# Kernel optimization log

Measured on AMD Instinct MI355X. Metric: run time of the kernel, lower is better.

## Reference

```python
import jax, jax.numpy as jnp
import numpy as np

ALPHA = 0.2          # LeakyReLU slope
NEG_BIG = -9e15      # mask value from the torch code
LN_EPS = 1e-5        # torch LayerNorm default eps
GAT_SCALE = 1.0


def _layer_norm(x, g, b):
    mu = x.mean(-1, keepdims=True)
    var = ((x - mu) ** 2).mean(-1, keepdims=True)
    return (x - mu) * jax.lax.rsqrt(var + LN_EPS) * g + b


def _gat_layer(h, adj, W, a, concat):
    # h: [B,N,Fin], adj: [N,N] weighted, W: [Fin,Fout], a: [2*Fout,1]
    Wh = jnp.einsum('bnf,fo->bno', h, W)                 # [B,N,Fout]
    Fo = W.shape[1]
    a_i, a_j = a[:Fo, 0], a[Fo:, 0]
    # e[b,i,j] = leakyrelu(Wh[b,i].a_i + Wh[b,j].a_j)  (== cat([Wh_i,Wh_j]) @ a)
    e = jax.nn.leaky_relu(
        (Wh @ a_i)[:, :, None] + (Wh @ a_j)[:, None, :], ALPHA)  # [B,N,N]
    att = jnp.where(adj[None, :, :] > 0, e, NEG_BIG)
    att = jax.nn.softmax(att, axis=2)
    att = att * adj[None, :, :]
    att = att / (att.sum(axis=2, keepdims=True) + 1e-8)
    h_prime = jnp.einsum('bij,bjo->bio', att, Wh)        # [B,N,Fout]
    return jax.nn.elu(h_prime) if concat else h_prime


def setup_inputs() -> dict:
    B, N, H, ID = 1024, 128, 64, 8
    GIN = 1 + ID  # node_feat_dim = 0
    key = jax.random.key(0)
    ks = jax.random.split(key, 20)
    # sparse weighted adjacency with self-loops
    w = jax.random.uniform(ks[0], (N, N))
    m = (jax.random.uniform(ks[1], (N, N)) < 0.3).astype(jnp.float32)
    adj = w * m + jnp.eye(N, dtype=jnp.float32)
    sc = lambda k, s: jax.random.normal(k, s, jnp.float32) * 0.1
    return {
        'c_values': jax.random.normal(ks[2], (B, N), jnp.float32),
        'adj': adj,
        'agent_emb': sc(ks[3], (N, ID)),
        'W1': sc(ks[4], (GIN, H)), 'a1': sc(ks[5], (2 * H, 1)),
        'W2': sc(ks[6], (H, H)),   'a2': sc(ks[7], (2 * H, 1)),
        'ln1_g': jnp.ones((H,)), 'ln1_b': jnp.zeros((H,)),
        'ln2_g': jnp.ones((H,)), 'ln2_b': jnp.zeros((H,)),
        'head_gat_w': sc(ks[8], (H, 1)), 'head_gat_b': jnp.zeros((1,)),
        'mlp1_w': sc(ks[9], (N, H)),  'mlp1_b': jnp.zeros((H,)),
        'mlp2_w': sc(ks[10], (H, H)), 'mlp2_b': jnp.zeros((H,)),
        'head_mlp_w': sc(ks[11], (H, 1)), 'head_mlp_b': jnp.zeros((1,)),
        'gate1_w': sc(ks[12], (N, H)), 'gate1_b': jnp.zeros((H,)),
        'gate2_w': sc(ks[13], (H, 1)), 'gate2_b': jnp.full((1,), -5.0),
    }


def reference(c_values, adj, agent_emb, W1, a1, W2, a2,
              ln1_g, ln1_b, ln2_g, ln2_b, head_gat_w, head_gat_b,
              mlp1_w, mlp1_b, mlp2_w, mlp2_b, head_mlp_w, head_mlp_b,
              gate1_w, gate1_b, gate2_w, gate2_b):
    B, N = c_values.shape
    # node features: [c_value, agent_id_embedding]
    id_feat = jnp.broadcast_to(agent_emb[None], (B, N, agent_emb.shape[1]))
    x_g = jnp.concatenate([c_values[..., None], id_feat], axis=-1)  # [B,N,9]
    h1 = _gat_layer(x_g, adj, W1, a1, concat=True)
    h1 = _layer_norm(h1, ln1_g, ln1_b)
    h2 = _gat_layer(h1, adj, W2, a2, concat=False)
    h = jax.nn.relu(h2 + h1)
    h = _layer_norm(h, ln2_g, ln2_b)
    q_gat = h.mean(axis=1) @ head_gat_w + head_gat_b                # [B,1]
    x_m = jax.nn.relu(c_values @ mlp1_w + mlp1_b)
    x_m = jax.nn.relu(x_m @ mlp2_w + mlp2_b)
    q_mlp = x_m @ head_mlp_w + head_mlp_b                           # [B,1]
    gate = jax.nn.sigmoid(
        jax.nn.relu(c_values @ gate1_w + gate1_b) @ gate2_w + gate2_b)
    return q_mlp + gate * GAT_SCALE * q_gat
```

## Files before the change

kernel.cpp:

```cpp
#include <hip/hip_runtime.h>
#include <hip/hip_bf16.h>

typedef unsigned short u16;
typedef unsigned int u32;
typedef short v8s __attribute__((ext_vector_type(8)));
typedef float v4f __attribute__((ext_vector_type(4)));

__device__ __forceinline__ float bflo(u32 d){union{u32 i;float f;}u;u.i=d<<16;return u.f;}
__device__ __forceinline__ float bfhi(u32 d){union{u32 i;float f;}u;u.i=d&0xffff0000u;return u.f;}
__device__ __forceinline__ u32 cvtpk(float a, float b){
    __hip_bfloat162 h = __float22bfloat162_rn(make_float2(a, b));
    u32 r; __builtin_memcpy(&r, &h, sizeof(r)); return r;
}
__device__ __forceinline__ v8s pack8(const float* w){
    union { uint4 u; v8s v; } c;
    c.u.x = cvtpk(w[0],w[1]); c.u.y = cvtpk(w[2],w[3]);
    c.u.z = cvtpk(w[4],w[5]); c.u.w = cvtpk(w[6],w[7]);
    return c.v;
}

__device__ __forceinline__ void flash_att(
    int wv, int l15, int q4,
    const float* __restrict__ ADJ,
    const float* __restrict__ sEi, const float* __restrict__ sFi,
    const float* __restrict__ sEj, const float* __restrict__ sFj,
    const u16* __restrict__ sWhT,
    v4f acc[2][4], v4f accD[2])
{
    const int r0 = 16*wv + l15, r1 = r0 + 64;
    const float Ei0 = sEi[r0], Fi0 = sFi[r0];
    const float Ei1 = sEi[r1], Fi1 = sFi[r1];
    const v8s ONES = {16256,16256,16256,16256,16256,16256,16256,16256};
    #pragma unroll
    for (int s = 0; s < 2; ++s) {
        accD[s] = (v4f){0.f,0.f,0.f,0.f};
        #pragma unroll
        for (int ct = 0; ct < 4; ++ct) acc[s][ct] = (v4f){0.f,0.f,0.f,0.f};
    }

    for (int ks = 0; ks < 4; ++ks) {
        const int ko = ks*32 + q4*8;
        float w0[8], w1[8];
        #pragma unroll
        for (int half = 0; half < 2; ++half) {
            float4 E4 = *(const float4*)(sEj + ko + 4*half);
            float4 F4 = *(const float4*)(sFj + ko + 4*half);
            float4 a0 = *(const float4*)(ADJ + r0*128 + ko + 4*half);
            float4 a1 = *(const float4*)(ADJ + r1*128 + ko + 4*half);
            float Ev[4] = {E4.x,E4.y,E4.z,E4.w};
            float Fv[4] = {F4.x,F4.y,F4.z,F4.w};
            float av0[4] = {a0.x,a0.y,a0.z,a0.w};
            float av1[4] = {a1.x,a1.y,a1.z,a1.w};
            #pragma unroll
            for (int k = 0; k < 4; ++k) {
                w0[half*4 + k] = fmaxf(Ei0*Ev[k], Fi0*Fv[k]) * av0[k];
                w1[half*4 + k] = fmaxf(Ei1*Ev[k], Fi1*Fv[k]) * av1[k];
            }
        }
        v8s A0 = pack8(w0), A1 = pack8(w1);
        accD[0] = __builtin_amdgcn_mfma_f32_16x16x32_bf16(ONES, A0, accD[0], 0,0,0);
        accD[1] = __builtin_amdgcn_mfma_f32_16x16x32_bf16(ONES, A1, accD[1], 0,0,0);
        #pragma unroll
        for (int ct = 0; ct < 4; ++ct) {
            v8s Wt = *(const v8s*)(sWhT + (16*ct + l15)*136 + ko);
            acc[0][ct] = __builtin_amdgcn_mfma_f32_16x16x32_bf16(Wt, A0, acc[0][ct], 0,0,0);
            acc[1][ct] = __builtin_amdgcn_mfma_f32_16x16x32_bf16(Wt, A1, acc[1][ct], 0,0,0);
        }
    }
}

__global__ __launch_bounds__(256, 4) void graphmixer_kernel(
    const float* __restrict__ C,
    const float* __restrict__ ADJ,
    const float* __restrict__ EMB,
    const float* __restrict__ W1,
    const float* __restrict__ A1,
    const float* __restrict__ W2,
    const float* __restrict__ A2,
    const float* __restrict__ LN1G, const float* __restrict__ LN1B,
    const float* __restrict__ LN2G, const float* __restrict__ LN2B,
    const float* __restrict__ HGW,  const float* __restrict__ HGB,
    const float* __restrict__ MLP1W, const float* __restrict__ MLP1B,
    const float* __restrict__ MLP2W, const float* __restrict__ MLP2B,
    const float* __restrict__ HMW,  const float* __restrict__ HMB,
    const float* __restrict__ G1W,  const float* __restrict__ G1B,
    const float* __restrict__ G2W,  const float* __restrict__ G2B,
    float* __restrict__ OUT)
{
    const int b = blockIdx.x, t = threadIdx.x;
    const int lane = t & 63, wv = t >> 6;
    const int l15 = lane & 15, q4 = lane >> 4;

    __shared__ __align__(16) unsigned char smem[21712];
    u16*   sWhT = (u16*)(smem);
    u16*   sH1  = (u16*)(smem);
    float* sEi  = (float*)(smem + 18432);
    float* sFi  = (float*)(smem + 18944);
    float* sEj  = (float*)(smem + 19456);
    float* sFj  = (float*)(smem + 19968);
    float* sScr = (float*)(smem + 20480);
    float* v2i  = (float*)(smem + 21056);
    float* v2j  = (float*)(smem + 21312);
    float* v1i  = (float*)(smem + 21568);
    float* v1j  = (float*)(smem + 21632);
    float* colp = (float*)(smem + 21696);

    const float* Cb = C + b*128;

    if (wv == 0) {
        if (lane >= 32 && lane < 41) {
            int f = lane - 32; float a0 = 0.f, a1 = 0.f;
            for (int q = 0; q < 16; q += 2) {
                float4 w = *(const float4*)(W1 + f*64 + q*4);
                float4 x = *(const float4*)(A1 + q*4);
                a0 += w.x*x.x + w.y*x.y + w.z*x.z + w.w*x.w;
                float4 w2 = *(const float4*)(W1 + f*64 + (q+1)*4);
                float4 x2 = *(const float4*)(A1 + (q+1)*4);
                a1 += w2.x*x2.x + w2.y*x2.y + w2.z*x2.z + w2.w*x2.w;
            }
            v1i[f] = a0 + a1;
        } else if (lane >= 48 && lane < 57) {
            int f = lane - 48; float a0 = 0.f, a1 = 0.f;
            for (int q = 0; q < 16; q += 2) {
                float4 w = *(const float4*)(W1 + f*64 + q*4);
                float4 x = *(const float4*)(A1 + 64 + q*4);
                a0 += w.x*x.x + w.y*x.y + w.z*x.z + w.w*x.w;
                float4 w2 = *(const float4*)(W1 + f*64 + (q+1)*4);
                float4 x2 = *(const float4*)(A1 + 64 + (q+1)*4);
                a1 += w2.x*x2.x + w2.y*x2.y + w2.z*x2.z + w2.w*x2.w;
            }
            v1j[f] = a0 + a1;
        }
    } else if (wv == 3) {
        float ai0 = 0.f, ai1 = 0.f, aj0 = 0.f, aj1 = 0.f;
        for (int q = 0; q < 16; ++q) {
            float4 w  = *(const float4*)(W2 + lane*64 + q*4);
            float4 xi = *(const float4*)(A2 + q*4);
            float4 xj = *(const float4*)(A2 + 64 + q*4);
            ai0 += w.x*xi.x + w.y*xi.y; ai1 += w.z*xi.z + w.w*xi.w;
            aj0 += w.x*xj.x + w.y*xj.y; aj1 += w.z*xj.z + w.w*xj.w;
        }
        v2i[lane] = ai0 + ai1; v2j[lane] = aj0 + aj1;
    } else if (wv == 1) {
        float a0 = 0.f, a1 = 0.f, a2v = 0.f, a3 = 0.f;
        for (int k = 0; k < 128; k += 4) {
            float4 c4 = *(const float4*)(Cb + k);
            a0  += c4.x*MLP1W[k*64+lane];
            a1  += c4.y*MLP1W[(k+1)*64+lane];
            a2v += c4.z*MLP1W[(k+2)*64+lane];
            a3  += c4.w*MLP1W[(k+3)*64+lane];
        }
        sScr[lane] = fmaxf(a0+a1+a2v+a3 + MLP1B[lane], 0.f);
        float b0 = 0.f, b1 = 0.f, b2 = 0.f, b3 = 0.f;
        for (int k = 0; k < 64; k += 4) {
            b0 += sScr[k]  *MLP2W[k*64 + lane];
            b1 += sScr[k+1]*MLP2W[(k+1)*64 + lane];
            b2 += sScr[k+2]*MLP2W[(k+2)*64 + lane];
            b3 += sScr[k+3]*MLP2W[(k+3)*64 + lane];
        }
        float x2 = fmaxf(b0+b1+b2+b3 + MLP2B[lane], 0.f);
        float p1 = x2 * HMW[lane];
        #pragma unroll
        for (int off = 32; off >= 1; off >>= 1) p1 += __shfl_down(p1, off);
        if (lane == 0) sScr[128] = p1 + HMB[0];
    } else {
        float a0 = 0.f, a1 = 0.f, a2v = 0.f, a3 = 0.f;
        for (int k = 0; k < 128; k += 4) {
            float4 c4 = *(const float4*)(Cb + k);
            a0  += c4.x*G1W[k*64+lane];
            a1  += c4.y*G1W[(k+1)*64+lane];
            a2v += c4.z*G1W[(k+2)*64+lane];
            a3  += c4.w*G1W[(k+3)*64+lane];
        }
        float g1 = fmaxf(a0+a1+a2v+a3 + G1B[lane], 0.f);
        float p2 = g1 * G2W[lane];
        #pragma unroll
        for (int off = 32; off >= 1; off >>= 1) p2 += __shfl_down(p2, off);
        if (lane == 0) sScr[129] = 1.f / (1.f + __expf(-(p2 + G2B[0])));
    }
    __syncthreads();

    {
        const int o = lane, cc = wv;
        float w1f[9];
        #pragma unroll
        for (int f = 0; f < 9; ++f) w1f[f] = W1[f*64 + o];
        float whv[32];
        for (int i = 0; i < 32; ++i) {
            const int ig = cc*32 + i;
            float a = Cb[ig] * w1f[0];
            float4 e0 = *(const float4*)(EMB + ig*8);
            float4 e1 = *(const float4*)(EMB + ig*8 + 4);
            a += e0.x*w1f[1] + e0.y*w1f[2] + e0.z*w1f[3] + e0.w*w1f[4];
            a += e1.x*w1f[5] + e1.y*w1f[6] + e1.z*w1f[7] + e1.w*w1f[8];
            whv[i] = a;
        }
        u32 p[16];
        #pragma unroll
        for (int q = 0; q < 16; ++q) p[q] = cvtpk(whv[2*q], whv[2*q+1]);
        uint4* dst = (uint4*)(sWhT + o*136 + cc*32);
        dst[0] = ((uint4*)p)[0]; dst[1] = ((uint4*)p)[1];
        dst[2] = ((uint4*)p)[2]; dst[3] = ((uint4*)p)[3];
    }
    if (t < 128) {
        float c = Cb[t];
        float4 e0 = *(const float4*)(EMB + t*8);
        float4 e1 = *(const float4*)(EMB + t*8 + 4);
        float ei = c*v1i[0] + e0.x*v1i[1]+e0.y*v1i[2]+e0.z*v1i[3]+e0.w*v1i[4]
                            + e1.x*v1i[5]+e1.y*v1i[6]+e1.z*v1i[7]+e1.w*v1i[8];
        float ej = c*v1j[0] + e0.x*v1j[1]+e0.y*v1j[2]+e0.z*v1j[3]+e0.w*v1j[4]
                            + e1.x*v1j[5]+e1.y*v1j[6]+e1.z*v1j[7]+e1.w*v1j[8];
        sEi[t] = __expf(ei); sFi[t] = __expf(0.2f*ei);
        sEj[t] = __expf(ej); sFj[t] = __expf(0.2f*ej);
    }
    __syncthreads();

    uint2 h1p[2][4];

    {
        v4f acc[2][4]; v4f accD[2];
        flash_att(wv, l15, q4, ADJ, sEi, sFi, sEj, sFj, sWhT, acc, accD);
        __syncthreads();

        float4 g4[4], b4[4], vi4[4], vj4[4];
        #pragma unroll
        for (int ct = 0; ct < 4; ++ct) {
            g4[ct] = *(const float4*)(LN1G + 16*ct + 4*q4);
            b4[ct] = *(const float4*)(LN1B + 16*ct + 4*q4);
            vi4[ct] = *(const float4*)(v2i + 16*ct + 4*q4);
            vj4[ct] = *(const float4*)(v2j + 16*ct + 4*q4);
        }
        #pragma unroll
        for (int s = 0; s < 2; ++s) {
            const int row = 16*wv + l15 + 64*s;
            const float rd = 1.f / accD[s][0];
            float x[4][4]; float s1 = 0.f, s2 = 0.f;
            #pragma unroll
            for (int ct = 0; ct < 4; ++ct) {
                #pragma unroll
                for (int reg = 0; reg < 4; ++reg) {
                    float v = acc[s][ct][reg] * rd;
                    v = (v > 0.f) ? v : (__expf(v) - 1.f);
                    x[ct][reg] = v;
                }
                s1 += (x[ct][0]+x[ct][1]) + (x[ct][2]+x[ct][3]);
                s2 += (x[ct][0]*x[ct][0]+x[ct][1]*x[ct][1])
                    + (x[ct][2]*x[ct][2]+x[ct][3]*x[ct][3]);
            }
            s1 += __shfl_xor(s1, 16); s2 += __shfl_xor(s2, 16);
            s1 += __shfl_xor(s1, 32); s2 += __shfl_xor(s2, 32);
            const float mean = s1 * (1.f/64.f);
            const float var  = s2 * (1.f/64.f) - mean*mean;
            const float rstd = rsqrtf(var + 1e-5f);
            float ei = 0.f, ej = 0.f;
            #pragma unroll
            for (int ct = 0; ct < 4; ++ct) {
                float h0 = (x[ct][0] - mean) * rstd * g4[ct].x + b4[ct].x;
                float h1 = (x[ct][1] - mean) * rstd * g4[ct].y + b4[ct].y;
                float h2 = (x[ct][2] - mean) * rstd * g4[ct].z + b4[ct].z;
                float h3 = (x[ct][3] - mean) * rstd * g4[ct].w + b4[ct].w;
                uint2 pw; pw.x = cvtpk(h0, h1); pw.y = cvtpk(h2, h3);
                h1p[s][ct] = pw;
                *(uint2*)(sH1 + row*72 + 16*ct + 4*q4) = pw;
                ei += h0*vi4[ct].x + h1*vi4[ct].y + h2*vi4[ct].z + h3*vi4[ct].w;
                ej += h0*vj4[ct].x + h1*vj4[ct].y + h2*vj4[ct].z + h3*vj4[ct].w;
            }
            ei += __shfl_xor(ei, 16); ei += __shfl_xor(ei, 32);
            ej += __shfl_xor(ej, 16); ej += __shfl_xor(ej, 32);
            if (q4 == 0) {
                sEi[row] = __expf(ei); sFi[row] = __expf(0.2f*ei);
                sEj[row] = __expf(ej); sFj[row] = __expf(0.2f*ej);
            }
        }
    }
    __syncthreads();

    {
        v8s Af[2][2];
        #pragma unroll
        for (int s = 0; s < 2; ++s)
            #pragma unroll
            for (int ks = 0; ks < 2; ++ks)
                Af[s][ks] = *(const v8s*)(sH1 + (16*(wv+4*s) + l15)*72 + ks*32 + q4*8);

        v4f acc2[2][4];
        #pragma unroll
        for (int s = 0; s < 2; ++s)
            #pragma unroll
            for (int ct = 0; ct < 4; ++ct) acc2[s][ct] = (v4f){0.f,0.f,0.f,0.f};
        #pragma unroll
        for (int ks = 0; ks < 2; ++ks) {
            const int kb = ks*32 + q4*8;
            #pragma unroll
            for (int ct = 0; ct < 4; ++ct) {
                const float* wp = W2 + kb*64 + 16*ct + l15;
                float w8[8];
                #pragma unroll
                for (int j = 0; j < 8; ++j) w8[j] = wp[j*64];
                v8s Bf = pack8(w8);
                #pragma unroll
                for (int s = 0; s < 2; ++s)
                    acc2[s][ct] = __builtin_amdgcn_mfma_f32_16x16x32_bf16(Af[s][ks], Bf, acc2[s][ct], 0,0,0);
            }
        }
        __syncthreads();
        #pragma unroll
        for (int s = 0; s < 2; ++s) {
            const int rb = 16*(wv+4*s) + 4*q4;
            #pragma unroll
            for (int ct = 0; ct < 4; ++ct) {
                const int col = 16*ct + l15;
                uint2 p;
                p.x = cvtpk(acc2[s][ct][0], acc2[s][ct][1]);
                p.y = cvtpk(acc2[s][ct][2], acc2[s][ct][3]);
                *(uint2*)(sWhT + col*136 + rb) = p;
            }
        }
    }
    __syncthreads();

    {
        v4f acc[2][4]; v4f accD[2];
        flash_att(wv, l15, q4, ADJ, sEi, sFi, sEj, sFj, sWhT, acc, accD);

        float4 g4[4], b4[4], hg4[4];
        #pragma unroll
        for (int ct = 0; ct < 4; ++ct) {
            g4[ct] = *(const float4*)(LN2G + 16*ct + 4*q4);
            b4[ct] = *(const float4*)(LN2B + 16*ct + 4*q4);
            hg4[ct] = *(const float4*)(HGW + 16*ct + 4*q4);
        }
        float ptot = 0.f;
        #pragma unroll
        for (int s = 0; s < 2; ++s) {
            const float rd = 1.f / accD[s][0];
            float x[4][4]; float s1 = 0.f, s2 = 0.f;
            #pragma unroll
            for (int ct = 0; ct < 4; ++ct) {
                const uint2 pw = h1p[s][ct];
                const float hv[4] = {bflo(pw.x), bfhi(pw.x), bflo(pw.y), bfhi(pw.y)};
                #pragma unroll
                for (int reg = 0; reg < 4; ++reg)
                    x[ct][reg] = fmaxf(acc[s][ct][reg] * rd + hv[reg], 0.f);
                s1 += (x[ct][0]+x[ct][1]) + (x[ct][2]+x[ct][3]);
                s2 += (x[ct][0]*x[ct][0]+x[ct][1]*x[ct][1])
                    + (x[ct][2]*x[ct][2]+x[ct][3]*x[ct][3]);
            }
            s1 += __shfl_xor(s1, 16); s2 += __shfl_xor(s2, 16);
            s1 += __shfl_xor(s1, 32); s2 += __shfl_xor(s2, 32);
            const float mean = s1 * (1.f/64.f);
            const float var  = s2 * (1.f/64.f) - mean*mean;
            const float rstd = rsqrtf(var + 1e-5f);
            #pragma unroll
            for (int ct = 0; ct < 4; ++ct) {
                float y0 = (x[ct][0] - mean) * rstd * g4[ct].x + b4[ct].x;
                float y1 = (x[ct][1] - mean) * rstd * g4[ct].y + b4[ct].y;
                float y2 = (x[ct][2] - mean) * rstd * g4[ct].z + b4[ct].z;
                float y3 = (x[ct][3] - mean) * rstd * g4[ct].w + b4[ct].w;
                ptot += y0*hg4[ct].x + y1*hg4[ct].y + y2*hg4[ct].z + y3*hg4[ct].w;
            }
        }
        ptot += __shfl_xor(ptot, 1);  ptot += __shfl_xor(ptot, 2);
        ptot += __shfl_xor(ptot, 4);  ptot += __shfl_xor(ptot, 8);
        ptot += __shfl_xor(ptot, 16); ptot += __shfl_xor(ptot, 32);
        if (lane == 0) colp[wv] = ptot;
    }
    __syncthreads();

    if (t == 0) {
        float s4 = (colp[0] + colp[1]) + (colp[2] + colp[3]);
        OUT[b] = sScr[128] + sScr[129] * (s4 * (1.f/128.f) + HGB[0]);
    }
}

extern "C" void kernel_launch(void* const* d_in, const int* in_sizes, int n_in,
                              void* d_out, int out_size, void* d_ws, size_t ws_size,
                              hipStream_t stream) {
    (void)n_in; (void)out_size; (void)d_ws; (void)ws_size;
    const float* C     = (const float*)d_in[0];
    const float* ADJ   = (const float*)d_in[1];
    const float* EMB   = (const float*)d_in[2];
    const float* W1    = (const float*)d_in[3];
    const float* A1    = (const float*)d_in[4];
    const float* W2    = (const float*)d_in[5];
    const float* A2    = (const float*)d_in[6];
    const float* LN1G  = (const float*)d_in[7];
    const float* LN1B  = (const float*)d_in[8];
    const float* LN2G  = (const float*)d_in[9];
    const float* LN2B  = (const float*)d_in[10];
    const float* HGW   = (const float*)d_in[11];
    const float* HGB   = (const float*)d_in[12];
    const float* MLP1W = (const float*)d_in[13];
    const float* MLP1B = (const float*)d_in[14];
    const float* MLP2W = (const float*)d_in[15];
    const float* MLP2B = (const float*)d_in[16];
    const float* HMW   = (const float*)d_in[17];
    const float* HMB   = (const float*)d_in[18];
    const float* G1W   = (const float*)d_in[19];
    const float* G1B   = (const float*)d_in[20];
    const float* G2W   = (const float*)d_in[21];
    const float* G2B   = (const float*)d_in[22];

    const int B = in_sizes[0] / 128;

    graphmixer_kernel<<<dim3(B), dim3(256), 0, stream>>>(
        C, ADJ, EMB, W1, A1, W2, A2, LN1G, LN1B, LN2G, LN2B,
        HGW, HGB, MLP1W, MLP1B, MLP2W, MLP2B, HMW, HMB,
        G1W, G1B, G2W, G2B, (float*)d_out);
}
```

Baseline: 138.9 us.

## Split GAT row tiles across eight waves and stage C/EMB in LDS

Doubles the block to 512 threads so each wave handles a single 16-row tile in both attention passes, the layer-1 projection and the W2 matmul, instead of two tiles per wave. Per-thread accumulator state is halved, which allows higher occupancy (launch bounds 512,7). The block's C row and the embedding table are copied into shared memory by otherwise idle waves, so the Wh and score computations no longer read them repeatedly from global memory. In exchange there are more barrier participants, larger shared memory use, and idle waves during the preamble.

Measured after the change: 165.0 us. 18.8% more time.

```diff
diff --git a/kernel.cpp b/kernel.cpp
--- a/kernel.cpp
+++ b/kernel.cpp
@@ -25,51 +25,41 @@
     const float* __restrict__ sEi, const float* __restrict__ sFi,
     const float* __restrict__ sEj, const float* __restrict__ sFj,
     const u16* __restrict__ sWhT,
-    v4f acc[2][4], v4f accD[2])
+    v4f acc[4], v4f* accD)
 {
-    const int r0 = 16*wv + l15, r1 = r0 + 64;
+    const int r0 = 16*wv + l15;
     const float Ei0 = sEi[r0], Fi0 = sFi[r0];
-    const float Ei1 = sEi[r1], Fi1 = sFi[r1];
     const v8s ONES = {16256,16256,16256,16256,16256,16256,16256,16256};
+    *accD = (v4f){0.f,0.f,0.f,0.f};
     #pragma unroll
-    for (int s = 0; s < 2; ++s) {
-        accD[s] = (v4f){0.f,0.f,0.f,0.f};
-        #pragma unroll
-        for (int ct = 0; ct < 4; ++ct) acc[s][ct] = (v4f){0.f,0.f,0.f,0.f};
-    }
+    for (int ct = 0; ct < 4; ++ct) acc[ct] = (v4f){0.f,0.f,0.f,0.f};
 
     for (int ks = 0; ks < 4; ++ks) {
         const int ko = ks*32 + q4*8;
-        float w0[8], w1[8];
+        float w0[8];
         #pragma unroll
         for (int half = 0; half < 2; ++half) {
             float4 E4 = *(const float4*)(sEj + ko + 4*half);
             float4 F4 = *(const float4*)(sFj + ko + 4*half);
             float4 a0 = *(const float4*)(ADJ + r0*128 + ko + 4*half);
-            float4 a1 = *(const float4*)(ADJ + r1*128 + ko + 4*half);
             float Ev[4] = {E4.x,E4.y,E4.z,E4.w};
             float Fv[4] = {F4.x,F4.y,F4.z,F4.w};
             float av0[4] = {a0.x,a0.y,a0.z,a0.w};
-            float av1[4] = {a1.x,a1.y,a1.z,a1.w};
             #pragma unroll
-            for (int k = 0; k < 4; ++k) {
+            for (int k = 0; k < 4; ++k)
                 w0[half*4 + k] = fmaxf(Ei0*Ev[k], Fi0*Fv[k]) * av0[k];
-                w1[half*4 + k] = fmaxf(Ei1*Ev[k], Fi1*Fv[k]) * av1[k];
-            }
-        }
-        v8s A0 = pack8(w0), A1 = pack8(w1);
-        accD[0] = __builtin_amdgcn_mfma_f32_16x16x32_bf16(ONES, A0, accD[0], 0,0,0);
-        accD[1] = __builtin_amdgcn_mfma_f32_16x16x32_bf16(ONES, A1, accD[1], 0,0,0);
+        }
+        v8s A0 = pack8(w0);
+        *accD = __builtin_amdgcn_mfma_f32_16x16x32_bf16(ONES, A0, *accD, 0,0,0);
         #pragma unroll
         for (int ct = 0; ct < 4; ++ct) {
             v8s Wt = *(const v8s*)(sWhT + (16*ct + l15)*136 + ko);
-            acc[0][ct] = __builtin_amdgcn_mfma_f32_16x16x32_bf16(Wt, A0, acc[0][ct], 0,0,0);
-            acc[1][ct] = __builtin_amdgcn_mfma_f32_16x16x32_bf16(Wt, A1, acc[1][ct], 0,0,0);
-        }
-    }
-}
-
-__global__ __launch_bounds__(256, 4) void graphmixer_kernel(
+            acc[ct] = __builtin_amdgcn_mfma_f32_16x16x32_bf16(Wt, A0, acc[ct], 0,0,0);
+        }
+    }
+}
+
+__global__ __launch_bounds__(512, 7) void graphmixer_kernel(
     const float* __restrict__ C,
     const float* __restrict__ ADJ,
     const float* __restrict__ EMB,
@@ -91,7 +81,7 @@
     const int lane = t & 63, wv = t >> 6;
     const int l15 = lane & 15, q4 = lane >> 4;
 
-    __shared__ __align__(16) unsigned char smem[21712];
+    __shared__ __align__(16) unsigned char smem[26336];
     u16*   sWhT = (u16*)(smem);
     u16*   sH1  = (u16*)(smem);
     float* sEi  = (float*)(smem + 18432);
@@ -104,6 +94,8 @@
     float* v1i  = (float*)(smem + 21568);
     float* v1j  = (float*)(smem + 21632);
     float* colp = (float*)(smem + 21696);
+    float* sC   = (float*)(smem + 21728);
+    float* sEmb = (float*)(smem + 22240);
 
     const float* Cb = C + b*128;
 
@@ -163,7 +155,7 @@
         #pragma unroll
         for (int off = 32; off >= 1; off >>= 1) p1 += __shfl_down(p1, off);
         if (lane == 0) sScr[128] = p1 + HMB[0];
-    } else {
+    } else if (wv == 2) {
         float a0 = 0.f, a1 = 0.f, a2v = 0.f, a3 = 0.f;
         for (int k = 0; k < 128; k += 4) {
             float4 c4 = *(const float4*)(Cb + k);
@@ -177,6 +169,12 @@
         #pragma unroll
         for (int off = 32; off >= 1; off >>= 1) p2 += __shfl_down(p2, off);
         if (lane == 0) sScr[129] = 1.f / (1.f + __expf(-(p2 + G2B[0])));
+    } else if (wv == 4) {
+        #pragma unroll
+        for (int q = 0; q < 4; ++q)
+            ((float4*)sEmb)[lane + 64*q] = ((const float4*)EMB)[lane + 64*q];
+    } else if (wv == 5) {
+        if (lane < 32) ((float4*)sC)[lane] = ((const float4*)Cb)[lane];
     }
     __syncthreads();
 
@@ -185,27 +183,27 @@
         float w1f[9];
         #pragma unroll
         for (int f = 0; f < 9; ++f) w1f[f] = W1[f*64 + o];
-        float whv[32];
-        for (int i = 0; i < 32; ++i) {
-            const int ig = cc*32 + i;
-            float a = Cb[ig] * w1f[0];
-            float4 e0 = *(const float4*)(EMB + ig*8);
-            float4 e1 = *(const float4*)(EMB + ig*8 + 4);
+        float whv[16];
+        #pragma unroll
+        for (int i = 0; i < 16; ++i) {
+            const int ig = cc*16 + i;
+            float a = sC[ig] * w1f[0];
+            float4 e0 = *(const float4*)(sEmb + ig*8);
+            float4 e1 = *(const float4*)(sEmb + ig*8 + 4);
             a += e0.x*w1f[1] + e0.y*w1f[2] + e0.z*w1f[3] + e0.w*w1f[4];
             a += e1.x*w1f[5] + e1.y*w1f[6] + e1.z*w1f[7] + e1.w*w1f[8];
             whv[i] = a;
         }
-        u32 p[16];
-        #pragma unroll
-        for (int q = 0; q < 16; ++q) p[q] = cvtpk(whv[2*q], whv[2*q+1]);
-        uint4* dst = (uint4*)(sWhT + o*136 + cc*32);
+        u32 p[8];
+        #pragma unroll
+        for (int q = 0; q < 8; ++q) p[q] = cvtpk(whv[2*q], whv[2*q+1]);
+        uint4* dst = (uint4*)(sWhT + o*136 + cc*16);
         dst[0] = ((uint4*)p)[0]; dst[1] = ((uint4*)p)[1];
-        dst[2] = ((uint4*)p)[2]; dst[3] = ((uint4*)p)[3];
     }
     if (t < 128) {
-        float c = Cb[t];
-        float4 e0 = *(const float4*)(EMB + t*8);
-        float4 e1 = *(const float4*)(EMB + t*8 + 4);
+        float c = sC[t];
+        float4 e0 = *(const float4*)(sEmb + t*8);
+        float4 e1 = *(const float4*)(sEmb + t*8 + 4);
         float ei = c*v1i[0] + e0.x*v1i[1]+e0.y*v1i[2]+e0.z*v1i[3]+e0.w*v1i[4]
                             + e1.x*v1i[5]+e1.y*v1i[6]+e1.z*v1i[7]+e1.w*v1i[8];
         float ej = c*v1j[0] + e0.x*v1j[1]+e0.y*v1j[2]+e0.z*v1j[3]+e0.w*v1j[4]
@@ -215,11 +213,11 @@
     }
     __syncthreads();
 
-    uint2 h1p[2][4];
+    uint2 h1p[4];
 
     {
-        v4f acc[2][4]; v4f accD[2];
-        flash_att(wv, l15, q4, ADJ, sEi, sFi, sEj, sFj, sWhT, acc, accD);
+        v4f acc[4]; v4f accD;
+        flash_att(wv, l15, q4, ADJ, sEi, sFi, sEj, sFj, sWhT, acc, &accD);
         __syncthreads();
 
         float4 g4[4], b4[4], vi4[4], vj4[4];
@@ -230,64 +228,57 @@
             vi4[ct] = *(const float4*)(v2i + 16*ct + 4*q4);
             vj4[ct] = *(const float4*)(v2j + 16*ct + 4*q4);
         }
-        #pragma unroll
-        for (int s = 0; s < 2; ++s) {
-            const int row = 16*wv + l15 + 64*s;
-            const float rd = 1.f / accD[s][0];
-            float x[4][4]; float s1 = 0.f, s2 = 0.f;
+        const int row = 16*wv + l15;
+        const float rd = 1.f / accD[0];
+        float x[4][4]; float s1 = 0.f, s2 = 0.f;
+        #pragma unroll
+        for (int ct = 0; ct < 4; ++ct) {
             #pragma unroll
-            for (int ct = 0; ct < 4; ++ct) {
-                #pragma unroll
-                for (int reg = 0; reg < 4; ++reg) {
-                    float v = acc[s][ct][reg] * rd;
-                    v = (v > 0.f) ? v : (__expf(v) - 1.f);
-                    x[ct][reg] = v;
-                }
-                s1 += (x[ct][0]+x[ct][1]) + (x[ct][2]+x[ct][3]);
-                s2 += (x[ct][0]*x[ct][0]+x[ct][1]*x[ct][1])
-                    + (x[ct][2]*x[ct][2]+x[ct][3]*x[ct][3]);
+            for (int reg = 0; reg < 4; ++reg) {
+                float v = acc[ct][reg] * rd;
+                v = (v > 0.f) ? v : (__expf(v) - 1.f);
+                x[ct][reg] = v;
             }
-            s1 += __shfl_xor(s1, 16); s2 += __shfl_xor(s2, 16);
-            s1 += __shfl_xor(s1, 32); s2 += __shfl_xor(s2, 32);
-            const float mean = s1 * (1.f/64.f);
-            const float var  = s2 * (1.f/64.f) - mean*mean;
-            const float rstd = rsqrtf(var + 1e-5f);
-            float ei = 0.f, ej = 0.f;
-            #pragma unroll
-            for (int ct = 0; ct < 4; ++ct) {
-                float h0 = (x[ct][0] - mean) * rstd * g4[ct].x + b4[ct].x;
-                float h1 = (x[ct][1] - mean) * rstd * g4[ct].y + b4[ct].y;
-                float h2 = (x[ct][2] - mean) * rstd * g4[ct].z + b4[ct].z;
-                float h3 = (x[ct][3] - mean) * rstd * g4[ct].w + b4[ct].w;
-                uint2 pw; pw.x = cvtpk(h0, h1); pw.y = cvtpk(h2, h3);
-                h1p[s][ct] = pw;
-                *(uint2*)(sH1 + row*72 + 16*ct + 4*q4) = pw;
-                ei += h0*vi4[ct].x + h1*vi4[ct].y + h2*vi4[ct].z + h3*vi4[ct].w;
-                ej += h0*vj4[ct].x + h1*vj4[ct].y + h2*vj4[ct].z + h3*vj4[ct].w;
-            }
-            ei += __shfl_xor(ei, 16); ei += __shfl_xor(ei, 32);
-            ej += __shfl_xor(ej, 16); ej += __shfl_xor(ej, 32);
-            if (q4 == 0) {
-                sEi[row] = __expf(ei); sFi[row] = __expf(0.2f*ei);
-                sEj[row] = __expf(ej); sFj[row] = __expf(0.2f*ej);
-            }
+            s1 += (x[ct][0]+x[ct][1]) + (x[ct][2]+x[ct][3]);
+            s2 += (x[ct][0]*x[ct][0]+x[ct][1]*x[ct][1])
+                + (x[ct][2]*x[ct][2]+x[ct][3]*x[ct][3]);
+        }
+        s1 += __shfl_xor(s1, 16); s2 += __shfl_xor(s2, 16);
+        s1 += __shfl_xor(s1, 32); s2 += __shfl_xor(s2, 32);
+        const float mean = s1 * (1.f/64.f);
+        const float var  = s2 * (1.f/64.f) - mean*mean;
+        const float rstd = rsqrtf(var + 1e-5f);
+        float ei = 0.f, ej = 0.f;
+        #pragma unroll
+        for (int ct = 0; ct < 4; ++ct) {
+            float h0 = (x[ct][0] - mean) * rstd * g4[ct].x + b4[ct].x;
+            float h1 = (x[ct][1] - mean) * rstd * g4[ct].y + b4[ct].y;
+            float h2 = (x[ct][2] - mean) * rstd * g4[ct].z + b4[ct].z;
+            float h3 = (x[ct][3] - mean) * rstd * g4[ct].w + b4[ct].w;
+            uint2 pw; pw.x = cvtpk(h0, h1); pw.y = cvtpk(h2, h3);
+            h1p[ct] = pw;
+            *(uint2*)(sH1 + row*72 + 16*ct + 4*q4) = pw;
+            ei += h0*vi4[ct].x + h1*vi4[ct].y + h2*vi4[ct].z + h3*vi4[ct].w;
+            ej += h0*vj4[ct].x + h1*vj4[ct].y + h2*vj4[ct].z + h3*vj4[ct].w;
+        }
+        ei += __shfl_xor(ei, 16); ei += __shfl_xor(ei, 32);
+        ej += __shfl_xor(ej, 16); ej += __shfl_xor(ej, 32);
+        if (q4 == 0) {
+            sEi[row] = __expf(ei); sFi[row] = __expf(0.2f*ei);
+            sEj[row] = __expf(ej); sFj[row] = __expf(0.2f*ej);
         }
     }
     __syncthreads();
 
     {
-        v8s Af[2][2];
-        #pragma unroll
-        for (int s = 0; s < 2; ++s)
-            #pragma unroll
-            for (int ks = 0; ks < 2; ++ks)
-                Af[s][ks] = *(const v8s*)(sH1 + (16*(wv+4*s) + l15)*72 + ks*32 + q4*8);
-
-        v4f acc2[2][4];
-        #pragma unroll
-        for (int s = 0; s < 2; ++s)
-            #pragma unroll
-            for (int ct = 0; ct < 4; ++ct) acc2[s][ct] = (v4f){0.f,0.f,0.f,0.f};
+        v8s Af[2];
+        #pragma unroll
+        for (int ks = 0; ks < 2; ++ks)
+            Af[ks] = *(const v8s*)(sH1 + (16*wv + l15)*72 + ks*32 + q4*8);
+
+        v4f acc2[4];
+        #pragma unroll
+        for (int ct = 0; ct < 4; ++ct) acc2[ct] = (v4f){0.f,0.f,0.f,0.f};
         #pragma unroll
         for (int ks = 0; ks < 2; ++ks) {
             const int kb = ks*32 + q4*8;
@@ -298,30 +289,25 @@
                 #pragma unroll
                 for (int j = 0; j < 8; ++j) w8[j] = wp[j*64];
                 v8s Bf = pack8(w8);
-                #pragma unroll
-                for (int s = 0; s < 2; ++s)
-                    acc2[s][ct] = __builtin_amdgcn_mfma_f32_16x16x32_bf16(Af[s][ks], Bf, acc2[s][ct], 0,0,0);
+                acc2[ct] = __builtin_amdgcn_mfma_f32_16x16x32_bf16(Af[ks], Bf, acc2[ct], 0,0,0);
             }
         }
         __syncthreads();
-        #pragma unroll
-        for (int s = 0; s < 2; ++s) {
-            const int rb = 16*(wv+4*s) + 4*q4;
-            #pragma unroll
-            for (int ct = 0; ct < 4; ++ct) {
-                const int col = 16*ct + l15;
-                uint2 p;
-                p.x = cvtpk(acc2[s][ct][0], acc2[s][ct][1]);
-                p.y = cvtpk(acc2[s][ct][2], acc2[s][ct][3]);
-                *(uint2*)(sWhT + col*136 + rb) = p;
-            }
+        const int rb = 16*wv + 4*q4;
+        #pragma unroll
+        for (int ct = 0; ct < 4; ++ct) {
+            const int col = 16*ct + l15;
+            uint2 p;
+            p.x = cvtpk(acc2[ct][0], acc2[ct][1]);
+            p.y = cvtpk(acc2[ct][2], acc2[ct][3]);
+            *(uint2*)(sWhT + col*136 + rb) = p;
         }
     }
     __syncthreads();
 
     {
-        v4f acc[2][4]; v4f accD[2];
-        flash_att(wv, l15, q4, ADJ, sEi, sFi, sEj, sFj, sWhT, acc, accD);
+        v4f acc[4]; v4f accD;
+        flash_att(wv, l15, q4, ADJ, sEi, sFi, sEj, sFj, sWhT, acc, &accD);
 
         float4 g4[4], b4[4], hg4[4];
         #pragma unroll
@@ -330,35 +316,32 @@
             b4[ct] = *(const float4*)(LN2B + 16*ct + 4*q4);
             hg4[ct] = *(const float4*)(HGW + 16*ct + 4*q4);
         }
+        const float rd = 1.f / accD[0];
+        float x[4][4]; float s1 = 0.f, s2 = 0.f;
+        #pragma unroll
+        for (int ct = 0; ct < 4; ++ct) {
+            const uint2 pw = h1p[ct];
+            const float hv[4] = {bflo(pw.x), bfhi(pw.x), bflo(pw.y), bfhi(pw.y)};
+            #pragma unroll
+            for (int reg = 0; reg < 4; ++reg)
+                x[ct][reg] = fmaxf(acc[ct][reg] * rd + hv[reg], 0.f);
+            s1 += (x[ct][0]+x[ct][1]) + (x[ct][2]+x[ct][3]);
+            s2 += (x[ct][0]*x[ct][0]+x[ct][1]*x[ct][1])
+                + (x[ct][2]*x[ct][2]+x[ct][3]*x[ct][3]);
+        }
+        s1 += __shfl_xor(s1, 16); s2 += __shfl_xor(s2, 16);
+        s1 += __shfl_xor(s1, 32); s2 += __shfl_xor(s2, 32);
+        const float mean = s1 * (1.f/64.f);
+        const float var  = s2 * (1.f/64.f) - mean*mean;
+        const float rstd = rsqrtf(var + 1e-5f);
         float ptot = 0.f;
         #pragma unroll
-        for (int s = 0; s < 2; ++s) {
-            const float rd = 1.f / accD[s][0];
-            float x[4][4]; float s1 = 0.f, s2 = 0.f;
-            #pragma unroll
-            for (int ct = 0; ct < 4; ++ct) {
-                const uint2 pw = h1p[s][ct];
-                const float hv[4] = {bflo(pw.x), bfhi(pw.x), bflo(pw.y), bfhi(pw.y)};
-                #pragma unroll
-                for (int reg = 0; reg < 4; ++reg)
-                    x[ct][reg] = fmaxf(acc[s][ct][reg] * rd + hv[reg], 0.f);
-                s1 += (x[ct][0]+x[ct][1]) + (x[ct][2]+x[ct][3]);
-                s2 += (x[ct][0]*x[ct][0]+x[ct][1]*x[ct][1])
-                    + (x[ct][2]*x[ct][2]+x[ct][3]*x[ct][3]);
-            }
-            s1 += __shfl_xor(s1, 16); s2 += __shfl_xor(s2, 16);
-            s1 += __shfl_xor(s1, 32); s2 += __shfl_xor(s2, 32);
-            const float mean = s1 * (1.f/64.f);
-            const float var  = s2 * (1.f/64.f) - mean*mean;
-            const float rstd = rsqrtf(var + 1e-5f);
-            #pragma unroll
-            for (int ct = 0; ct < 4; ++ct) {
-                float y0 = (x[ct][0] - mean) * rstd * g4[ct].x + b4[ct].x;
-                float y1 = (x[ct][1] - mean) * rstd * g4[ct].y + b4[ct].y;
-                float y2 = (x[ct][2] - mean) * rstd * g4[ct].z + b4[ct].z;
-                float y3 = (x[ct][3] - mean) * rstd * g4[ct].w + b4[ct].w;
-                ptot += y0*hg4[ct].x + y1*hg4[ct].y + y2*hg4[ct].z + y3*hg4[ct].w;
-            }
+        for (int ct = 0; ct < 4; ++ct) {
+            float y0 = (x[ct][0] - mean) * rstd * g4[ct].x + b4[ct].x;
+            float y1 = (x[ct][1] - mean) * rstd * g4[ct].y + b4[ct].y;
+            float y2 = (x[ct][2] - mean) * rstd * g4[ct].z + b4[ct].z;
+            float y3 = (x[ct][3] - mean) * rstd * g4[ct].w + b4[ct].w;
+            ptot += y0*hg4[ct].x + y1*hg4[ct].y + y2*hg4[ct].z + y3*hg4[ct].w;
         }
         ptot += __shfl_xor(ptot, 1);  ptot += __shfl_xor(ptot, 2);
         ptot += __shfl_xor(ptot, 4);  ptot += __shfl_xor(ptot, 8);
@@ -368,7 +351,8 @@
     __syncthreads();
 
     if (t == 0) {
-        float s4 = (colp[0] + colp[1]) + (colp[2] + colp[3]);
+        float s4 = ((colp[0] + colp[1]) + (colp[2] + colp[3]))
+                 + ((colp[4] + colp[5]) + (colp[6] + colp[7]));
         OUT[b] = sScr[128] + sScr[129] * (s4 * (1.f/128.f) + HGB[0]);
     }
 }
@@ -403,7 +387,7 @@
 
     const int B = in_sizes[0] / 128;
 
-    graphmixer_kernel<<<dim3(B), dim3(256), 0, stream>>>(
+    graphmixer_kernel<<<dim3(B), dim3(512), 0, stream>>>(
         C, ADJ, EMB, W1, A1, W2, A2, LN1G, LN1B, LN2G, LN2B,
         HGW, HGB, MLP1W, MLP1B, MLP2W, MLP2B, HMW, HMB,
         G1W, G1B, G2W, G2B, (float*)d_out);
```

## Process two batch samples per 512-thread block sharing adjacency row loads

Applied to the files above, without the earlier changes.

Each block now handles two batch elements with eight waves, and each wave computes one row tile for both samples. A single adjacency row load feeds both samples' attention weights, halving ADJ reads per sample. C and the agent embedding are staged in LDS. The cost is more LDS per block (about 47 KB vs 21 KB) and half as many blocks (512), which may reduce occupancy and the number of blocks available to spread across CUs.

Result: faster. 130.2 us (-6.3%).

```diff
diff --git a/kernel.cpp b/kernel.cpp
--- a/kernel.cpp
+++ b/kernel.cpp
@@ -19,17 +19,16 @@
     return c.v;
 }
 
-__device__ __forceinline__ void flash_att(
+__device__ __forceinline__ void flash_att2(
     int wv, int l15, int q4,
     const float* __restrict__ ADJ,
-    const float* __restrict__ sEi, const float* __restrict__ sFi,
-    const float* __restrict__ sEj, const float* __restrict__ sFj,
-    const u16* __restrict__ sWhT,
+    const float* __restrict__ expb,
+    const u16* __restrict__ whtb,
     v4f acc[2][4], v4f accD[2])
 {
-    const int r0 = 16*wv + l15, r1 = r0 + 64;
-    const float Ei0 = sEi[r0], Fi0 = sFi[r0];
-    const float Ei1 = sEi[r1], Fi1 = sFi[r1];
+    const int r0 = 16*wv + l15;
+    const float Ei0 = expb[r0],       Fi0 = expb[128 + r0];
+    const float Ei1 = expb[512 + r0], Fi1 = expb[640 + r0];
     const v8s ONES = {16256,16256,16256,16256,16256,16256,16256,16256};
     #pragma unroll
     for (int s = 0; s < 2; ++s) {
@@ -43,18 +42,20 @@
         float w0[8], w1[8];
         #pragma unroll
         for (int half = 0; half < 2; ++half) {
-            float4 E4 = *(const float4*)(sEj + ko + 4*half);
-            float4 F4 = *(const float4*)(sFj + ko + 4*half);
-            float4 a0 = *(const float4*)(ADJ + r0*128 + ko + 4*half);
-            float4 a1 = *(const float4*)(ADJ + r1*128 + ko + 4*half);
-            float Ev[4] = {E4.x,E4.y,E4.z,E4.w};
-            float Fv[4] = {F4.x,F4.y,F4.z,F4.w};
-            float av0[4] = {a0.x,a0.y,a0.z,a0.w};
-            float av1[4] = {a1.x,a1.y,a1.z,a1.w};
+            float4 E0 = *(const float4*)(expb + 256 + ko + 4*half);
+            float4 F0 = *(const float4*)(expb + 384 + ko + 4*half);
+            float4 E1 = *(const float4*)(expb + 768 + ko + 4*half);
+            float4 F1 = *(const float4*)(expb + 896 + ko + 4*half);
+            float4 a  = *(const float4*)(ADJ + r0*128 + ko + 4*half);
+            float Ev0[4] = {E0.x,E0.y,E0.z,E0.w};
+            float Fv0[4] = {F0.x,F0.y,F0.z,F0.w};
+            float Ev1[4] = {E1.x,E1.y,E1.z,E1.w};
+            float Fv1[4] = {F1.x,F1.y,F1.z,F1.w};
+            float av[4]  = {a.x,a.y,a.z,a.w};
             #pragma unroll
             for (int k = 0; k < 4; ++k) {
-                w0[half*4 + k] = fmaxf(Ei0*Ev[k], Fi0*Fv[k]) * av0[k];
-                w1[half*4 + k] = fmaxf(Ei1*Ev[k], Fi1*Fv[k]) * av1[k];
+                w0[half*4 + k] = fmaxf(Ei0*Ev0[k], Fi0*Fv0[k]) * av[k];
+                w1[half*4 + k] = fmaxf(Ei1*Ev1[k], Fi1*Fv1[k]) * av[k];
             }
         }
         v8s A0 = pack8(w0), A1 = pack8(w1);
@@ -62,14 +63,15 @@
         accD[1] = __builtin_amdgcn_mfma_f32_16x16x32_bf16(ONES, A1, accD[1], 0,0,0);
         #pragma unroll
         for (int ct = 0; ct < 4; ++ct) {
-            v8s Wt = *(const v8s*)(sWhT + (16*ct + l15)*136 + ko);
-            acc[0][ct] = __builtin_amdgcn_mfma_f32_16x16x32_bf16(Wt, A0, acc[0][ct], 0,0,0);
-            acc[1][ct] = __builtin_amdgcn_mfma_f32_16x16x32_bf16(Wt, A1, acc[1][ct], 0,0,0);
+            v8s Wt0 = *(const v8s*)(whtb + (16*ct + l15)*136 + ko);
+            v8s Wt1 = *(const v8s*)(whtb + 9216 + (16*ct + l15)*136 + ko);
+            acc[0][ct] = __builtin_amdgcn_mfma_f32_16x16x32_bf16(Wt0, A0, acc[0][ct], 0,0,0);
+            acc[1][ct] = __builtin_amdgcn_mfma_f32_16x16x32_bf16(Wt1, A1, acc[1][ct], 0,0,0);
         }
     }
 }
 
-__global__ __launch_bounds__(256, 4) void graphmixer_kernel(
+__global__ __launch_bounds__(512, 4) void graphmixer_kernel(
     const float* __restrict__ C,
     const float* __restrict__ ADJ,
     const float* __restrict__ EMB,
@@ -87,25 +89,25 @@
     const float* __restrict__ G2W,  const float* __restrict__ G2B,
     float* __restrict__ OUT)
 {
-    const int b = blockIdx.x, t = threadIdx.x;
+    const int blk = blockIdx.x, t = threadIdx.x;
     const int lane = t & 63, wv = t >> 6;
     const int l15 = lane & 15, q4 = lane >> 4;
 
-    __shared__ __align__(16) unsigned char smem[21712];
-    u16*   sWhT = (u16*)(smem);
-    u16*   sH1  = (u16*)(smem);
-    float* sEi  = (float*)(smem + 18432);
-    float* sFi  = (float*)(smem + 18944);
-    float* sEj  = (float*)(smem + 19456);
-    float* sFj  = (float*)(smem + 19968);
-    float* sScr = (float*)(smem + 20480);
-    float* v2i  = (float*)(smem + 21056);
-    float* v2j  = (float*)(smem + 21312);
-    float* v1i  = (float*)(smem + 21568);
-    float* v1j  = (float*)(smem + 21632);
-    float* colp = (float*)(smem + 21696);
-
-    const float* Cb = C + b*128;
+    __shared__ __align__(16) unsigned char smem[47936];
+    u16*   R1   = (u16*)(smem);
+    float* expb = (float*)(smem + 36864);
+    float* sScr0= (float*)(smem + 40960);
+    float* sScr1= (float*)(smem + 41536);
+    float* v2i  = (float*)(smem + 42112);
+    float* v2j  = (float*)(smem + 42368);
+    float* v1i  = (float*)(smem + 42624);
+    float* v1j  = (float*)(smem + 42688);
+    float* colp = (float*)(smem + 42752);
+    float* sC   = (float*)(smem + 42816);
+    float* sEmb = (float*)(smem + 43840);
+
+    const float* Cb0 = C + (2*blk)*128;
+    const float* Cb1 = C + (2*blk+1)*128;
 
     if (wv == 0) {
         if (lane >= 32 && lane < 41) {
@@ -141,7 +143,9 @@
             aj0 += w.x*xj.x + w.y*xj.y; aj1 += w.z*xj.z + w.w*xj.w;
         }
         v2i[lane] = ai0 + ai1; v2j[lane] = aj0 + aj1;
-    } else if (wv == 1) {
+    } else if (wv == 1 || wv == 4) {
+        const float* Cb = (wv == 1) ? Cb0 : Cb1;
+        float* sScr = (wv == 1) ? sScr0 : sScr1;
         float a0 = 0.f, a1 = 0.f, a2v = 0.f, a3 = 0.f;
         for (int k = 0; k < 128; k += 4) {
             float4 c4 = *(const float4*)(Cb + k);
@@ -163,7 +167,9 @@
         #pragma unroll
         for (int off = 32; off >= 1; off >>= 1) p1 += __shfl_down(p1, off);
         if (lane == 0) sScr[128] = p1 + HMB[0];
-    } else {
+    } else if (wv == 2 || wv == 5) {
+        const float* Cb = (wv == 2) ? Cb0 : Cb1;
+        float* sScr = (wv == 2) ? sScr0 : sScr1;
         float a0 = 0.f, a1 = 0.f, a2v = 0.f, a3 = 0.f;
         for (int k = 0; k < 128; k += 4) {
             float4 c4 = *(const float4*)(Cb + k);
@@ -177,6 +183,13 @@
         #pragma unroll
         for (int off = 32; off >= 1; off >>= 1) p2 += __shfl_down(p2, off);
         if (lane == 0) sScr[129] = 1.f / (1.f + __expf(-(p2 + G2B[0])));
+    } else if (wv == 6) {
+        #pragma unroll
+        for (int q = 0; q < 4; ++q)
+            ((float4*)sEmb)[lane + 64*q] = ((const float4*)EMB)[lane + 64*q];
+    } else {
+        if (lane < 32)       ((float4*)sC)[lane] = ((const float4*)Cb0)[lane];
+        else                 ((float4*)(sC+128))[lane-32] = ((const float4*)Cb1)[lane-32];
     }
     __syncthreads();
 
@@ -185,33 +198,40 @@
         float w1f[9];
         #pragma unroll
         for (int f = 0; f < 9; ++f) w1f[f] = W1[f*64 + o];
-        float whv[32];
-        for (int i = 0; i < 32; ++i) {
-            const int ig = cc*32 + i;
-            float a = Cb[ig] * w1f[0];
-            float4 e0 = *(const float4*)(EMB + ig*8);
-            float4 e1 = *(const float4*)(EMB + ig*8 + 4);
-            a += e0.x*w1f[1] + e0.y*w1f[2] + e0.z*w1f[3] + e0.w*w1f[4];
-            a += e1.x*w1f[5] + e1.y*w1f[6] + e1.z*w1f[7] + e1.w*w1f[8];
-            whv[i] = a;
-        }
-        u32 p[16];
-        #pragma unroll
-        for (int q = 0; q < 16; ++q) p[q] = cvtpk(whv[2*q], whv[2*q+1]);
-        uint4* dst = (uint4*)(sWhT + o*136 + cc*32);
-        dst[0] = ((uint4*)p)[0]; dst[1] = ((uint4*)p)[1];
-        dst[2] = ((uint4*)p)[2]; dst[3] = ((uint4*)p)[3];
-    }
-    if (t < 128) {
-        float c = Cb[t];
-        float4 e0 = *(const float4*)(EMB + t*8);
-        float4 e1 = *(const float4*)(EMB + t*8 + 4);
+        #pragma unroll
+        for (int s = 0; s < 2; ++s) {
+            const float* cs = sC + s*128;
+            float whv[16];
+            #pragma unroll
+            for (int i = 0; i < 16; ++i) {
+                const int ig = cc*16 + i;
+                float a = cs[ig] * w1f[0];
+                float4 e0 = *(const float4*)(sEmb + ig*8);
+                float4 e1 = *(const float4*)(sEmb + ig*8 + 4);
+                a += e0.x*w1f[1] + e0.y*w1f[2] + e0.z*w1f[3] + e0.w*w1f[4];
+                a += e1.x*w1f[5] + e1.y*w1f[6] + e1.z*w1f[7] + e1.w*w1f[8];
+                whv[i] = a;
+            }
+            u32 p[8];
+            #pragma unroll
+            for (int q = 0; q < 8; ++q) p[q] = cvtpk(whv[2*q], whv[2*q+1]);
+            uint4* dst = (uint4*)(R1 + s*9216 + o*136 + cc*16);
+            dst[0] = ((uint4*)p)[0]; dst[1] = ((uint4*)p)[1];
+        }
+    }
+    if (t < 256) {
+        const int s = t >> 7, row = t & 127;
+        const float* cs = sC + s*128;
+        float c = cs[row];
+        float4 e0 = *(const float4*)(sEmb + row*8);
+        float4 e1 = *(const float4*)(sEmb + row*8 + 4);
         float ei = c*v1i[0] + e0.x*v1i[1]+e0.y*v1i[2]+e0.z*v1i[3]+e0.w*v1i[4]
                             + e1.x*v1i[5]+e1.y*v1i[6]+e1.z*v1i[7]+e1.w*v1i[8];
         float ej = c*v1j[0] + e0.x*v1j[1]+e0.y*v1j[2]+e0.z*v1j[3]+e0.w*v1j[4]
                             + e1.x*v1j[5]+e1.y*v1j[6]+e1.z*v1j[7]+e1.w*v1j[8];
-        sEi[t] = __expf(ei); sFi[t] = __expf(0.2f*ei);
-        sEj[t] = __expf(ej); sFj[t] = __expf(0.2f*ej);
+        float* eb = expb + s*512;
+        eb[row]       = __expf(ei); eb[128 + row] = __expf(0.2f*ei);
+        eb[256 + row] = __expf(ej); eb[384 + row] = __expf(0.2f*ej);
     }
     __syncthreads();
 
@@ -219,7 +239,7 @@
 
     {
         v4f acc[2][4]; v4f accD[2];
-        flash_att(wv, l15, q4, ADJ, sEi, sFi, sEj, sFj, sWhT, acc, accD);
+        flash_att2(wv, l15, q4, ADJ, expb, R1, acc, accD);
         __syncthreads();
 
         float4 g4[4], b4[4], vi4[4], vj4[4];
@@ -230,9 +250,9 @@
             vi4[ct] = *(const float4*)(v2i + 16*ct + 4*q4);
             vj4[ct] = *(const float4*)(v2j + 16*ct + 4*q4);
         }
+        const int row = 16*wv + l15;
         #pragma unroll
         for (int s = 0; s < 2; ++s) {
-            const int row = 16*wv + l15 + 64*s;
             const float rd = 1.f / accD[s][0];
             float x[4][4]; float s1 = 0.f, s2 = 0.f;
             #pragma unroll
@@ -253,6 +273,7 @@
             const float var  = s2 * (1.f/64.f) - mean*mean;
             const float rstd = rsqrtf(var + 1e-5f);
             float ei = 0.f, ej = 0.f;
+            u16* h1s = R1 + s*9216;
             #pragma unroll
             for (int ct = 0; ct < 4; ++ct) {
                 float h0 = (x[ct][0] - mean) * rstd * g4[ct].x + b4[ct].x;
@@ -261,15 +282,16 @@
                 float h3 = (x[ct][3] - mean) * rstd * g4[ct].w + b4[ct].w;
                 uint2 pw; pw.x = cvtpk(h0, h1); pw.y = cvtpk(h2, h3);
                 h1p[s][ct] = pw;
-                *(uint2*)(sH1 + row*72 + 16*ct + 4*q4) = pw;
+                *(uint2*)(h1s + row*72 + 16*ct + 4*q4) = pw;
                 ei += h0*vi4[ct].x + h1*vi4[ct].y + h2*vi4[ct].z + h3*vi4[ct].w;
                 ej += h0*vj4[ct].x + h1*vj4[ct].y + h2*vj4[ct].z + h3*vj4[ct].w;
             }
             ei += __shfl_xor(ei, 16); ei += __shfl_xor(ei, 32);
             ej += __shfl_xor(ej, 16); ej += __shfl_xor(ej, 32);
             if (q4 == 0) {
-                sEi[row] = __expf(ei); sFi[row] = __expf(0.2f*ei);
-                sEj[row] = __expf(ej); sFj[row] = __expf(0.2f*ej);
+                float* eb = expb + s*512;
+                eb[row]       = __expf(ei); eb[128 + row] = __expf(0.2f*ei);
+                eb[256 + row] = __expf(ej); eb[384 + row] = __expf(0.2f*ej);
             }
         }
     }
@@ -281,7 +303,7 @@
         for (int s = 0; s < 2; ++s)
             #pragma unroll
             for (int ks = 0; ks < 2; ++ks)
-                Af[s][ks] = *(const v8s*)(sH1 + (16*(wv+4*s) + l15)*72 + ks*32 + q4*8);
+                Af[s][ks] = *(const v8s*)(R1 + s*9216 + (16*wv + l15)*72 + ks*32 + q4*8);
 
         v4f acc2[2][4];
         #pragma unroll
@@ -298,22 +320,22 @@
                 #pragma unroll
                 for (int j = 0; j < 8; ++j) w8[j] = wp[j*64];
                 v8s Bf = pack8(w8);
-                #pragma unroll
-                for (int s = 0; s < 2; ++s)
-                    acc2[s][ct] = __builtin_amdgcn_mfma_f32_16x16x32_bf16(Af[s][ks], Bf, acc2[s][ct], 0,0,0);
+                acc2[0][ct] = __builtin_amdgcn_mfma_f32_16x16x32_bf16(Af[0][ks], Bf, acc2[0][ct], 0,0,0);
+                acc2[1][ct] = __builtin_amdgcn_mfma_f32_16x16x32_bf16(Af[1][ks], Bf, acc2[1][ct], 0,0,0);
             }
         }
         __syncthreads();
+        const int rb = 16*wv + 4*q4;
         #pragma unroll
         for (int s = 0; s < 2; ++s) {
-            const int rb = 16*(wv+4*s) + 4*q4;
+            u16* wt = R1 + s*9216;
             #pragma unroll
             for (int ct = 0; ct < 4; ++ct) {
                 const int col = 16*ct + l15;
                 uint2 p;
                 p.x = cvtpk(acc2[s][ct][0], acc2[s][ct][1]);
                 p.y = cvtpk(acc2[s][ct][2], acc2[s][ct][3]);
-                *(uint2*)(sWhT + col*136 + rb) = p;
+                *(uint2*)(wt + col*136 + rb) = p;
             }
         }
     }
@@ -321,7 +343,7 @@
 
     {
         v4f acc[2][4]; v4f accD[2];
-        flash_att(wv, l15, q4, ADJ, sEi, sFi, sEj, sFj, sWhT, acc, accD);
+        flash_att2(wv, l15, q4, ADJ, expb, R1, acc, accD);
 
         float4 g4[4], b4[4], hg4[4];
         #pragma unroll
@@ -330,7 +352,6 @@
             b4[ct] = *(const float4*)(LN2B + 16*ct + 4*q4);
             hg4[ct] = *(const float4*)(HGW + 16*ct + 4*q4);
         }
-        float ptot = 0.f;
         #pragma unroll
         for (int s = 0; s < 2; ++s) {
             const float rd = 1.f / accD[s][0];
@@ -351,6 +372,7 @@
             const float mean = s1 * (1.f/64.f);
             const float var  = s2 * (1.f/64.f) - mean*mean;
             const float rstd = rsqrtf(var + 1e-5f);
+            float ptot = 0.f;
             #pragma unroll
             for (int ct = 0; ct < 4; ++ct) {
                 float y0 = (x[ct][0] - mean) * rstd * g4[ct].x + b4[ct].x;
@@ -359,17 +381,22 @@
                 float y3 = (x[ct][3] - mean) * rstd * g4[ct].w + b4[ct].w;
                 ptot += y0*hg4[ct].x + y1*hg4[ct].y + y2*hg4[ct].z + y3*hg4[ct].w;
             }
-        }
-        ptot += __shfl_xor(ptot, 1);  ptot += __shfl_xor(ptot, 2);
-        ptot += __shfl_xor(ptot, 4);  ptot += __shfl_xor(ptot, 8);
-        ptot += __shfl_xor(ptot, 16); ptot += __shfl_xor(ptot, 32);
-        if (lane == 0) colp[wv] = ptot;
+            ptot += __shfl_xor(ptot, 1);  ptot += __shfl_xor(ptot, 2);
+            ptot += __shfl_xor(ptot, 4);  ptot += __shfl_xor(ptot, 8);
+            ptot += __shfl_xor(ptot, 16); ptot += __shfl_xor(ptot, 32);
+            if (lane == 0) colp[s*8 + wv] = ptot;
+        }
     }
     __syncthreads();
 
     if (t == 0) {
-        float s4 = (colp[0] + colp[1]) + (colp[2] + colp[3]);
-        OUT[b] = sScr[128] + sScr[129] * (s4 * (1.f/128.f) + HGB[0]);
+        float hgb = HGB[0];
+        float s0 = ((colp[0] + colp[1]) + (colp[2] + colp[3]))
+                 + ((colp[4] + colp[5]) + (colp[6] + colp[7]));
+        OUT[2*blk]   = sScr0[128] + sScr0[129] * (s0 * (1.f/128.f) + hgb);
+        float s1 = ((colp[8] + colp[9]) + (colp[10] + colp[11]))
+                 + ((colp[12] + colp[13]) + (colp[14] + colp[15]));
+        OUT[2*blk+1] = sScr1[128] + sScr1[129] * (s1 * (1.f/128.f) + hgb);
     }
 }
 
@@ -403,7 +430,7 @@
 
     const int B = in_sizes[0] / 128;
 
-    graphmixer_kernel<<<dim3(B), dim3(256), 0, stream>>>(
+    graphmixer_kernel<<<dim3(B/2), dim3(512), 0, stream>>>(
         C, ADJ, EMB, W1, A1, W2, A2, LN1G, LN1B, LN2G, LN2B,
         HGW, HGB, MLP1W, MLP1B, MLP2W, MLP2B, HMW, HMB,
         G1W, G1B, G2W, G2B, (float*)d_out);
```
